# Kernel optimization log

Hardware: AMD Instinct MI355X
Metric: run time of the kernel (lower is better)

## Reference

```python
import jax, jax.numpy as jnp
import numpy as np

EMBED_DIM = 1024
NUM_HEADS = 16
HEAD_DIM = EMBED_DIM // NUM_HEADS
B, S = 8, 1024


def setup_inputs() -> dict:
    key = jax.random.key(0)
    k1, k2, k3, k4, k5 = jax.random.split(key, 5)
    scale_in = 1.0 / np.sqrt(EMBED_DIM)
    return {
        "qkv": jax.random.normal(k1, (B, S, EMBED_DIM), dtype=jnp.float32),
        "w_in": jax.random.normal(k2, (3 * EMBED_DIM, EMBED_DIM), dtype=jnp.float32) * scale_in,
        "b_in": jax.random.normal(k3, (3 * EMBED_DIM,), dtype=jnp.float32) * 0.01,
        "w_out": jax.random.normal(k4, (EMBED_DIM, EMBED_DIM), dtype=jnp.float32) * scale_in,
        "b_out": jax.random.normal(k5, (EMBED_DIM,), dtype=jnp.float32) * 0.01,
    }


def reference(qkv, w_in, b_in, w_out, b_out):
    # in_proj: [B,S,E] -> [B,S,3E]  (torch Linear: x @ W.T + b)
    proj = qkv @ w_in.T + b_in
    q, k, v = jnp.split(proj, 3, axis=2)
    # split heads: [B,S,E] -> [B,S,H,D]
    def heads(t):
        return t.reshape(B, S, NUM_HEADS, HEAD_DIM)
    q, k, v = heads(q), heads(k), heads(v)
    # scaled dot-product attention per head; scale = sqrt(head_dim)
    scores = jnp.einsum("bqhd,bkhd->bhqk", q, k) / jnp.sqrt(jnp.float32(HEAD_DIM))
    attn = jax.nn.softmax(scores, axis=-1)
    out = jnp.einsum("bhqk,bkhd->bqhd", attn, v)  # [B,S,H,D]
    out = out.reshape(B, S, EMBED_DIM)  # concat heads along feature dim
    return out @ w_out.T + b_out
```

## Files before the change

kernel.cpp:

```cpp
#include <hip/hip_runtime.h>

typedef _Float16 f16;
typedef _Float16 f16x4 __attribute__((ext_vector_type(4)));
typedef _Float16 f16x8 __attribute__((ext_vector_type(8)));
typedef float f32x4 __attribute__((ext_vector_type(4)));
typedef float f32x16 __attribute__((ext_vector_type(16)));
typedef unsigned u32x4 __attribute__((ext_vector_type(4)));

#define DEVINL __device__ __forceinline__
#define VMCNT(n) asm volatile("s_waitcnt vmcnt(" #n ")" ::: "memory")

DEVINL void gload16(const void* g, void* l) {
    __builtin_amdgcn_global_load_lds(
        (const __attribute__((address_space(1))) unsigned int*)g,
        (__attribute__((address_space(3))) unsigned int*)l, 16, 0, 0);
}

DEVINL unsigned pk2(float a, float b) {
    auto v = __builtin_amdgcn_cvt_pkrtz(a, b);
    return __builtin_bit_cast(unsigned, v);
}

__global__ __launch_bounds__(256) void cvt_kernel(const float* __restrict__ in,
                                                  f16* __restrict__ out, int n4) {
    int i = blockIdx.x * 256 + threadIdx.x;
    int st = gridDim.x * 256;
    for (; i < n4; i += st) {
        float4 v = reinterpret_cast<const float4*>(in)[i];
        f16x4 o = {(f16)v.x, (f16)v.y, (f16)v.z, (f16)v.w};
        reinterpret_cast<f16x4*>(out)[i] = o;
    }
}

__global__ __launch_bounds__(256) void gemm_in(const f16* __restrict__ A,
                                               const f16* __restrict__ Bm,
                                               const float* __restrict__ bias,
                                               f16* __restrict__ Qw, f16* __restrict__ Kw,
                                               f16* __restrict__ Vtw) {
    constexpr int K = 1024, NT = K / 32;
    __shared__ f16 As[2][128 * 32];
    __shared__ f16 Bs[2][128 * 32];
    const int t = threadIdx.x;
    const int wave = t >> 6, lane = t & 63, lr = lane & 15, lg = lane >> 4;
    const int wr = wave >> 1, wc = wave & 1;
    const int m0 = blockIdx.y * 128, n0 = blockIdx.x * 128;

    const f16* Ag = A + (m0 + (t >> 2)) * K + (t & 3) * 8;
    const f16* Bg = Bm + (n0 + (t >> 2)) * K + (t & 3) * 8;

    f32x4 acc[4][4] = {};

    auto stage = [&](int buf, int kt) {
        const f16* a = Ag + kt * 32;
        const f16* b = Bg + kt * 32;
        f16* al = &As[buf][t * 8];
        f16* bl = &Bs[buf][t * 8];
        gload16(a, al);
        gload16(a + 64 * K, al + 64 * 32);
        gload16(b, bl);
        gload16(b + 64 * K, bl + 64 * 32);
    };

    stage(0, 0);
    __syncthreads();
    int cur = 0;
    for (int kt = 0; kt < NT; ++kt) {
        if (kt + 1 < NT) stage(cur ^ 1, kt + 1);
        const f16* as = &As[cur][0];
        const f16* bs = &Bs[cur][0];
        f16x8 af[4], bf[4];
#pragma unroll
        for (int i = 0; i < 4; ++i)
            af[i] = *(const f16x8*)&as[(wr * 64 + i * 16 + lr) * 32 + lg * 8];
#pragma unroll
        for (int i = 0; i < 4; ++i)
            bf[i] = *(const f16x8*)&bs[(wc * 64 + i * 16 + lr) * 32 + lg * 8];
#pragma unroll
        for (int i = 0; i < 4; ++i)
#pragma unroll
            for (int j = 0; j < 4; ++j)
                acc[i][j] = __builtin_amdgcn_mfma_f32_16x16x32_f16(af[i], bf[j], acc[i][j], 0, 0, 0);
        __syncthreads();
        cur ^= 1;
    }

    const float SCQ = 0.18033688011112042f;
#pragma unroll
    for (int nf = 0; nf < 4; ++nf) {
        int n = n0 + wc * 64 + nf * 16 + lr;
        float bv = bias[n];
        int part = n >> 10, e = n & 1023, hh = e >> 6, dd = e & 63;
#pragma unroll
        for (int mf = 0; mf < 4; ++mf) {
            int m = m0 + wr * 64 + mf * 16 + lg * 4;
            int bb = m >> 10, ss = m & 1023;
            if (part == 0) {
                f16* dst = Qw + ((bb * 16 + hh) * 1024 + ss) * 64 + dd;
#pragma unroll
                for (int r = 0; r < 4; ++r) dst[r * 64] = (f16)((acc[mf][nf][r] + bv) * SCQ);
            } else if (part == 1) {
                f16* dst = Kw + ((bb * 16 + hh) * 1024 + ss) * 64 + dd;
#pragma unroll
                for (int r = 0; r < 4; ++r) dst[r * 64] = (f16)(acc[mf][nf][r] + bv);
            } else {
                f16x4 pkv;
#pragma unroll
                for (int r = 0; r < 4; ++r) pkv[r] = (f16)(acc[mf][nf][r] + bv);
                *(f16x4*)(Vtw + ((bb * 16 + hh) * 64 + dd) * 1024 + ss) = pkv;
            }
        }
    }
}

__global__ __launch_bounds__(256) void gemm_out(const f16* __restrict__ A,
                                                const f16* __restrict__ Bm,
                                                const float* __restrict__ bias,
                                                float* __restrict__ Cout) {
    constexpr int K = 1024, NT = K / 32;
    __shared__ f16 As[2][128 * 32];
    __shared__ f16 Bs[2][128 * 32];
    const int t = threadIdx.x;
    const int wave = t >> 6, lane = t & 63, lr = lane & 15, lg = lane >> 4;
    const int wr = wave >> 1, wc = wave & 1;
    const int m0 = blockIdx.y * 128, n0 = blockIdx.x * 128;

    const f16* Ag = A + (m0 + (t >> 2)) * K + (t & 3) * 8;
    const f16* Bg = Bm + (n0 + (t >> 2)) * K + (t & 3) * 8;

    f32x4 acc[4][4] = {};

    auto stage = [&](int buf, int kt) {
        const f16* a = Ag + kt * 32;
        const f16* b = Bg + kt * 32;
        f16* al = &As[buf][t * 8];
        f16* bl = &Bs[buf][t * 8];
        gload16(a, al);
        gload16(a + 64 * K, al + 64 * 32);
        gload16(b, bl);
        gload16(b + 64 * K, bl + 64 * 32);
    };

    stage(0, 0);
    __syncthreads();
    int cur = 0;
    for (int kt = 0; kt < NT; ++kt) {
        if (kt + 1 < NT) stage(cur ^ 1, kt + 1);
        const f16* as = &As[cur][0];
        const f16* bs = &Bs[cur][0];
        f16x8 af[4], bf[4];
#pragma unroll
        for (int i = 0; i < 4; ++i)
            af[i] = *(const f16x8*)&as[(wr * 64 + i * 16 + lr) * 32 + lg * 8];
#pragma unroll
        for (int i = 0; i < 4; ++i)
            bf[i] = *(const f16x8*)&bs[(wc * 64 + i * 16 + lr) * 32 + lg * 8];
#pragma unroll
        for (int i = 0; i < 4; ++i)
#pragma unroll
            for (int j = 0; j < 4; ++j)
                acc[i][j] = __builtin_amdgcn_mfma_f32_16x16x32_f16(af[i], bf[j], acc[i][j], 0, 0, 0);
        __syncthreads();
        cur ^= 1;
    }
#pragma unroll
    for (int nf = 0; nf < 4; ++nf) {
        int n = n0 + wc * 64 + nf * 16 + lr;
        float bv = bias[n];
#pragma unroll
        for (int mf = 0; mf < 4; ++mf) {
            int m = m0 + wr * 64 + mf * 16 + lg * 4;
#pragma unroll
            for (int r = 0; r < 4; ++r) Cout[(m + r) * 1024 + n] = acc[mf][nf][r] + bv;
        }
    }
}

__global__ __launch_bounds__(512, 2) void attn_kernel(const f16* __restrict__ Qw,
                                                      const f16* __restrict__ Kw,
                                                      const f16* __restrict__ Vtw,
                                                      f16* __restrict__ AO) {
    __shared__ char LDSb[65536];
    const int t = threadIdx.x, wave = t >> 6, lane = t & 63;
    const int ql = lane & 31, hi = lane >> 5;
    const int wg = blockIdx.x;
    const int gid = (wg & 7) * 64 + (wg >> 3);
    const int qt = gid & 3, h = (gid >> 2) & 15, b = gid >> 6;
    const f16* Qp = Qw + (b * 16 + h) * 1024 * 64;
    const f16* Kp = Kw + (b * 16 + h) * 1024 * 64;
    const f16* Vp = Vtw + (b * 16 + h) * 64 * 1024;
    const int q0 = qt * 256 + wave * 32;

    f16x8 qb[4];
#pragma unroll
    for (int s = 0; s < 4; ++s)
        qb[s] = *(const f16x8*)&Qp[(q0 + ql) * 64 + s * 16 + hi * 8];

    const int srow = t >> 3;
    const int gw = ((t & 7) << 4) ^ ((srow & 7) << 4);
    auto stage_kv = [&](int slot, int kv) {
        gload16((const char*)(Kp + (kv + srow) * 64) + gw, LDSb + slot * 8192 + t * 16);
        gload16((const char*)(Vp + srow * 1024 + kv) + gw, LDSb + 32768 + slot * 8192 + t * 16);
    };

    f32x16 o0 = 0.f, o1 = 0.f;
    float mraw = -1e30f, lsum = 0.f;

    stage_kv(0, 0);
    stage_kv(1, 64);
    stage_kv(2, 128);
    VMCNT(4);

    for (int kv = 0; kv < 16; ++kv) {
        __builtin_amdgcn_s_barrier();
        if (kv + 3 < 16) stage_kv((kv + 3) & 3, (kv + 3) * 64);
        const char* Kb = LDSb + (kv & 3) * 8192;
        const char* Vb = LDSb + 32768 + (kv & 3) * 8192;

        f32x16 st0, st1;
        __builtin_amdgcn_s_setprio(1);
#pragma unroll
        for (int s = 0; s < 4; ++s) {
            int byt = (s * 32 + hi * 16) ^ ((ql & 7) << 4);
            f16x8 k0 = *(const f16x8*)(Kb + ql * 128 + byt);
            f16x8 k1 = *(const f16x8*)(Kb + (32 + ql) * 128 + byt);
            if (s == 0) {
                st0 = __builtin_amdgcn_mfma_f32_32x32x16_f16(k0, qb[0], (f32x16)0.f, 0, 0, 0);
                st1 = __builtin_amdgcn_mfma_f32_32x32x16_f16(k1, qb[0], (f32x16)0.f, 0, 0, 0);
            } else {
                st0 = __builtin_amdgcn_mfma_f32_32x32x16_f16(k0, qb[s], st0, 0, 0, 0);
                st1 = __builtin_amdgcn_mfma_f32_32x32x16_f16(k1, qb[s], st1, 0, 0, 0);
            }
        }
        __builtin_amdgcn_s_setprio(0);

        float a[16];
#pragma unroll
        for (int r = 0; r < 16; ++r) a[r] = fmaxf(st0[r], st1[r]);
#pragma unroll
        for (int s = 8; s >= 1; s >>= 1)
#pragma unroll
            for (int r = 0; r < 16; ++r)
                if (r < s) a[r] = fmaxf(a[r], a[r + s]);
        float mx = fmaxf(a[0], __shfl_xor(a[0], 32, 64));

        if (__all(mx <= mraw + 8.f)) {
#pragma unroll
            for (int r = 0; r < 16; ++r) st0[r] = exp2f(st0[r] - mraw);
#pragma unroll
            for (int r = 0; r < 16; ++r) st1[r] = exp2f(st1[r] - mraw);
            float sa[16];
#pragma unroll
            for (int r = 0; r < 16; ++r) sa[r] = st0[r] + st1[r];
#pragma unroll
            for (int s = 8; s >= 1; s >>= 1)
#pragma unroll
                for (int r = 0; r < 16; ++r)
                    if (r < s) sa[r] += sa[r + s];
            lsum += sa[0] + __shfl_xor(sa[0], 32, 64);
        } else {
            float mn = fmaxf(mraw, mx);
            float al = exp2f(mraw - mn);
            mraw = mn;
#pragma unroll
            for (int r = 0; r < 16; ++r) st0[r] = exp2f(st0[r] - mn);
#pragma unroll
            for (int r = 0; r < 16; ++r) st1[r] = exp2f(st1[r] - mn);
            float sa[16];
#pragma unroll
            for (int r = 0; r < 16; ++r) sa[r] = st0[r] + st1[r];
#pragma unroll
            for (int s = 8; s >= 1; s >>= 1)
#pragma unroll
                for (int r = 0; r < 16; ++r)
                    if (r < s) sa[r] += sa[r + s];
            lsum = lsum * al + sa[0] + __shfl_xor(sa[0], 32, 64);
            o0 *= al;
            o1 *= al;
        }

#pragma unroll
        for (int s = 0; s < 4; ++s) {
            const int s1 = s & 1;
            float p0, p1, p2, p3, p4, p5, p6, p7;
            if (s < 2) {
                p0 = st0[8 * s1 + 0]; p1 = st0[8 * s1 + 1]; p2 = st0[8 * s1 + 2]; p3 = st0[8 * s1 + 3];
                p4 = st0[8 * s1 + 4]; p5 = st0[8 * s1 + 5]; p6 = st0[8 * s1 + 6]; p7 = st0[8 * s1 + 7];
            } else {
                p0 = st1[8 * s1 + 0]; p1 = st1[8 * s1 + 1]; p2 = st1[8 * s1 + 2]; p3 = st1[8 * s1 + 3];
                p4 = st1[8 * s1 + 4]; p5 = st1[8 * s1 + 5]; p6 = st1[8 * s1 + 6]; p7 = st1[8 * s1 + 7];
            }
            unsigned c0 = pk2(p0, p1), c1 = pk2(p2, p3);
            unsigned c2 = pk2(p4, p5), c3 = pk2(p6, p7);
            unsigned y0 = __shfl_xor(hi ? c0 : c2, 32, 64);
            unsigned y1 = __shfl_xor(hi ? c1 : c3, 32, 64);
            unsigned w0 = hi ? y0 : c0;
            unsigned w1 = hi ? y1 : c1;
            unsigned w2 = hi ? c2 : y0;
            unsigned w3 = hi ? c3 : y1;
            u32x4 pw = {w0, w1, w2, w3};
            f16x8 pf = __builtin_bit_cast(f16x8, pw);
            __builtin_amdgcn_s_setprio(1);
#pragma unroll
            for (int db = 0; db < 2; ++db) {
                int row = db * 32 + ql;
                int byt = (s * 32 + hi * 16) ^ ((row & 7) << 4);
                f16x8 vf = *(const f16x8*)(Vb + row * 128 + byt);
                if (db == 0)
                    o0 = __builtin_amdgcn_mfma_f32_32x32x16_f16(vf, pf, o0, 0, 0, 0);
                else
                    o1 = __builtin_amdgcn_mfma_f32_32x32x16_f16(vf, pf, o1, 0, 0, 0);
            }
            __builtin_amdgcn_s_setprio(0);
        }
        if (kv <= 12) VMCNT(4);
        else if (kv == 13) VMCNT(2);
        else if (kv == 14) VMCNT(0);
    }

    __syncthreads();
    float inv = 1.0f / lsum;
    char* obase = LDSb + wave * 4096;
#pragma unroll
    for (int db = 0; db < 2; ++db)
#pragma unroll
        for (int r = 0; r < 16; ++r) {
            int d = db * 32 + (r & 3) + 8 * (r >> 2) + 4 * hi;
            float v = (db == 0 ? o0[r] : o1[r]) * inv;
            *(f16*)(obase + ql * 128 + ((2 * d) ^ ((ql & 7) << 4))) = (f16)v;
        }
    __syncthreads();
    const int rl = lane >> 1, c4 = (lane & 1) * 4;
#pragma unroll
    for (int i = 0; i < 4; ++i) {
        f16x8 ov = *(const f16x8*)(obase + rl * 128 + (((c4 + i) * 16) ^ ((rl & 7) << 4)));
        *(f16x8*)&AO[(b * 1024 + q0 + rl) * 1024 + h * 64 + (c4 + i) * 8] = ov;
    }
}

extern "C" void kernel_launch(void* const* d_in, const int* in_sizes, int n_in,
                              void* d_out, int out_size, void* d_ws, size_t ws_size,
                              hipStream_t stream) {
    const float* qkv = (const float*)d_in[0];
    const float* w_in = (const float*)d_in[1];
    const float* b_in = (const float*)d_in[2];
    const float* w_out = (const float*)d_in[3];
    const float* b_out = (const float*)d_in[4];
    float* out = (float*)d_out;

    f16* Xh = (f16*)d_ws;
    f16* Wih = Xh + 8388608;
    f16* Woh = Wih + 3145728;
    f16* Qw = Woh + 1048576;
    f16* Kw = Qw + 8388608;
    f16* Vtw = Kw + 8388608;
    f16* AO = Xh;

    cvt_kernel<<<2048, 256, 0, stream>>>(qkv, Xh, 8388608 / 4);
    cvt_kernel<<<1024, 256, 0, stream>>>(w_in, Wih, 3145728 / 4);
    cvt_kernel<<<512, 256, 0, stream>>>(w_out, Woh, 1048576 / 4);

    gemm_in<<<dim3(24, 64), 256, 0, stream>>>(Xh, Wih, b_in, Qw, Kw, Vtw);
    attn_kernel<<<512, 512, 0, stream>>>(Qw, Kw, Vtw, AO);
    gemm_out<<<dim3(8, 64), 256, 0, stream>>>(AO, Woh, b_out, out);
}
```

Before: 285.8 us.

## Swizzle GEMM tile order across XCDs and shrink attention blocks to four waves

Both GEMMs switch to a 1D grid with an XCD-aware swizzle, so that neighbouring tiles which share A/B panels land on the same chiplet and reuse its L2. The attention kernel halves its workgroup to 256 threads (128 queries per block) and doubles the grid. Each thread now stages two K/V rows per tile, so the vmcnt thresholds are doubled to match. Scheduling barriers are added around the loop, and the post-loop __syncthreads is dropped because the epilogue only writes LDS regions no wave still reads. The risk is that with 64KB of LDS per block, the smaller blocks may give fewer resident waves per CU than before.

```diff
diff --git a/kernel.cpp b/kernel.cpp
--- a/kernel.cpp
+++ b/kernel.cpp
@@ -9,6 +9,7 @@
 
 #define DEVINL __device__ __forceinline__
 #define VMCNT(n) asm volatile("s_waitcnt vmcnt(" #n ")" ::: "memory")
+#define SCHEDBAR() __builtin_amdgcn_sched_barrier(0)
 
 DEVINL void gload16(const void* g, void* l) {
     __builtin_amdgcn_global_load_lds(
@@ -43,7 +44,9 @@
     const int t = threadIdx.x;
     const int wave = t >> 6, lane = t & 63, lr = lane & 15, lg = lane >> 4;
     const int wr = wave >> 1, wc = wave & 1;
-    const int m0 = blockIdx.y * 128, n0 = blockIdx.x * 128;
+    const int wg = blockIdx.x;
+    const int swz = (wg & 7) * 192 + (wg >> 3);
+    const int m0 = (swz / 24) * 128, n0 = (swz % 24) * 128;
 
     const f16* Ag = A + (m0 + (t >> 2)) * K + (t & 3) * 8;
     const f16* Bg = Bm + (n0 + (t >> 2)) * K + (t & 3) * 8;
@@ -122,7 +125,9 @@
     const int t = threadIdx.x;
     const int wave = t >> 6, lane = t & 63, lr = lane & 15, lg = lane >> 4;
     const int wr = wave >> 1, wc = wave & 1;
-    const int m0 = blockIdx.y * 128, n0 = blockIdx.x * 128;
+    const int wg = blockIdx.x;
+    const int swz = (wg & 7) * 64 + (wg >> 3);
+    const int m0 = (swz / 8) * 128, n0 = (swz % 8) * 128;
 
     const f16* Ag = A + (m0 + (t >> 2)) * K + (t & 3) * 8;
     const f16* Bg = Bm + (n0 + (t >> 2)) * K + (t & 3) * 8;
@@ -175,31 +180,38 @@
     }
 }
 
-__global__ __launch_bounds__(512, 2) void attn_kernel(const f16* __restrict__ Qw,
-                                                      const f16* __restrict__ Kw,
-                                                      const f16* __restrict__ Vtw,
-                                                      f16* __restrict__ AO) {
+__global__ __launch_bounds__(256) void attn_kernel(const f16* __restrict__ Qw,
+                                                   const f16* __restrict__ Kw,
+                                                   const f16* __restrict__ Vtw,
+                                                   f16* __restrict__ AO) {
     __shared__ char LDSb[65536];
     const int t = threadIdx.x, wave = t >> 6, lane = t & 63;
     const int ql = lane & 31, hi = lane >> 5;
     const int wg = blockIdx.x;
-    const int gid = (wg & 7) * 64 + (wg >> 3);
-    const int qt = gid & 3, h = (gid >> 2) & 15, b = gid >> 6;
+    const int gid = (wg & 7) * 128 + (wg >> 3);
+    const int qt = gid & 7, h = (gid >> 3) & 15, b = gid >> 7;
     const f16* Qp = Qw + (b * 16 + h) * 1024 * 64;
     const f16* Kp = Kw + (b * 16 + h) * 1024 * 64;
     const f16* Vp = Vtw + (b * 16 + h) * 64 * 1024;
-    const int q0 = qt * 256 + wave * 32;
+    const int q0 = qt * 128 + wave * 32;
 
     f16x8 qb[4];
 #pragma unroll
     for (int s = 0; s < 4; ++s)
         qb[s] = *(const f16x8*)&Qp[(q0 + ql) * 64 + s * 16 + hi * 8];
 
-    const int srow = t >> 3;
-    const int gw = ((t & 7) << 4) ^ ((srow & 7) << 4);
+    const int srow0 = t >> 3;
+    const int sw = (t & 7) << 4;
     auto stage_kv = [&](int slot, int kv) {
-        gload16((const char*)(Kp + (kv + srow) * 64) + gw, LDSb + slot * 8192 + t * 16);
-        gload16((const char*)(Vp + srow * 1024 + kv) + gw, LDSb + 32768 + slot * 8192 + t * 16);
+#pragma unroll
+        for (int c = 0; c < 2; ++c) {
+            int row = c * 32 + srow0;
+            int gwb = sw ^ ((row & 7) << 4);
+            gload16((const char*)(Kp + (kv + row) * 64) + gwb,
+                    LDSb + slot * 8192 + c * 4096 + t * 16);
+            gload16((const char*)(Vp + row * 1024 + kv) + gwb,
+                    LDSb + 32768 + slot * 8192 + c * 4096 + t * 16);
+        }
     };
 
     f32x16 o0 = 0.f, o1 = 0.f;
@@ -208,10 +220,11 @@
     stage_kv(0, 0);
     stage_kv(1, 64);
     stage_kv(2, 128);
-    VMCNT(4);
+    VMCNT(8);
 
     for (int kv = 0; kv < 16; ++kv) {
         __builtin_amdgcn_s_barrier();
+        SCHEDBAR();
         if (kv + 3 < 16) stage_kv((kv + 3) & 3, (kv + 3) * 64);
         const char* Kb = LDSb + (kv & 3) * 8192;
         const char* Vb = LDSb + 32768 + (kv & 3) * 8192;
@@ -312,12 +325,13 @@
             }
             __builtin_amdgcn_s_setprio(0);
         }
-        if (kv <= 12) VMCNT(4);
-        else if (kv == 13) VMCNT(2);
+        if (kv <= 12) VMCNT(8);
+        else if (kv == 13) VMCNT(4);
         else if (kv == 14) VMCNT(0);
-    }
-
-    __syncthreads();
+        SCHEDBAR();
+    }
+
+    SCHEDBAR();
     float inv = 1.0f / lsum;
     char* obase = LDSb + wave * 4096;
 #pragma unroll
@@ -359,7 +373,7 @@
     cvt_kernel<<<1024, 256, 0, stream>>>(w_in, Wih, 3145728 / 4);
     cvt_kernel<<<512, 256, 0, stream>>>(w_out, Woh, 1048576 / 4);
 
-    gemm_in<<<dim3(24, 64), 256, 0, stream>>>(Xh, Wih, b_in, Qw, Kw, Vtw);
-    attn_kernel<<<512, 512, 0, stream>>>(Qw, Kw, Vtw, AO);
-    gemm_out<<<dim3(8, 64), 256, 0, stream>>>(AO, Woh, b_out, out);
-}
+    gemm_in<<<1536, 256, 0, stream>>>(Xh, Wih, b_in, Qw, Kw, Vtw);
+    attn_kernel<<<1024, 256, 0, stream>>>(Qw, Kw, Vtw, AO);
+    gemm_out<<<512, 256, 0, stream>>>(AO, Woh, b_out, out);
+}
```

New measurement: 300.3 us. 5.1% more time.
